# Optimization experiments

Hardware: AMD Instinct MI355X
Metric: run time of the kernel (lower is better)

## Reference

```python
import jax, jax.numpy as jnp
import numpy as np

N_HEADS = 16


def setup_inputs() -> dict:
    key = jax.random.key(0)
    ks = jax.random.split(key, 9)
    B, S, D = 4, 2048, 1024
    query = jax.random.normal(ks[0], (B, S, D), dtype=jnp.float32)
    key_t = jax.random.normal(ks[1], (B, S, D), dtype=jnp.float32)
    value = jax.random.normal(ks[2], (B, S, D), dtype=jnp.float32)
    mask = jax.random.randint(ks[3], (B, 1, S, S), 0, 10) > 0
    scale_w = 0.02  # keep exp(attention) in a safe range
    Wq = jax.random.normal(ks[4], (D, D), dtype=jnp.float32) * scale_w
    Wk = jax.random.normal(ks[5], (D, D), dtype=jnp.float32) * scale_w
    Wv = jax.random.normal(ks[6], (D, D), dtype=jnp.float32) * scale_w
    fc_w = jax.random.normal(ks[7], (D, D), dtype=jnp.float32) * scale_w
    fc_b = jnp.zeros((D,), dtype=jnp.float32)
    return {"query": query, "key": key_t, "value": value, "mask": mask,
            "Wq": Wq, "Wk": Wk, "Wv": Wv, "fc_w": fc_w, "fc_b": fc_b}


def reference(query, key, value, mask, Wq, Wk, Wv, fc_w, fc_b):
    B, S, D = query.shape
    H = N_HEADS
    Dh = D // H
    scale = jnp.sqrt(jnp.asarray(D / H, dtype=query.dtype))
    # Faithful to original: direct reshape [B,S,D] -> [B,H,S,Dh] (no transpose)
    Q = (query @ Wq.T).reshape(B, H, S, Dh)
    K = (key @ Wk.T).reshape(B, H, S, Dh)
    V = (value @ Wv.T).reshape(B, H, S, Dh)
    attn = jnp.einsum('bhqd,bhkd->bhqk', Q, K) / scale  # [B,H,S,S]
    # Hand-rolled masked softmax: exp, masked_fill(False->0), normalize, nan->0
    temp = jnp.where(mask, jnp.exp(attn), 0.0)
    attn = temp / jnp.sum(temp, axis=-1, keepdims=True)
    attn = jnp.where(jnp.isnan(attn), 0.0, attn)
    res = jnp.einsum('bhqk,bhkd->bhqd', attn, V)  # [B,H,S,Dh]
    outs = res.transpose(0, 2, 1, 3).reshape(B, S, D)
    outs = outs @ fc_w.T + fc_b
    return outs, res.transpose(1, 0, 2, 3)
```

## Files before the change

### kernel.cpp

```cpp
#include <hip/hip_runtime.h>


typedef __attribute__((ext_vector_type(8))) short bf16x8;
typedef __attribute__((ext_vector_type(4))) short bf16x4;
typedef __attribute__((ext_vector_type(4))) float f32x4;

#define MFMA32(a, b, c) __builtin_amdgcn_mfma_f32_16x16x32_bf16(a, b, c, 0, 0, 0)

static __device__ __forceinline__ float fast_exp2(float x) {
#if __has_builtin(__builtin_amdgcn_exp2f)
  return __builtin_amdgcn_exp2f(x);
#else
  return __expf(x * 0.69314718056f);
#endif
}

__device__ __forceinline__ unsigned short fbf(float f) {
  union { float f; unsigned u; } x; x.f = f;
  unsigned r = x.u + 0x7fffu + ((x.u >> 16) & 1u);
  return (unsigned short)(r >> 16);
}

static __device__ __forceinline__ bf16x4 pack2(unsigned lo, unsigned hi) {
  union { unsigned u[2]; bf16x4 v; } x; x.u[0] = lo; x.u[1] = hi; return x.v;
}

static __device__ __forceinline__ bf16x8 cat2(bf16x4 lo, bf16x4 hi) {
  union { bf16x4 h[2]; bf16x8 v; } x; x.h[0] = lo; x.h[1] = hi; return x.v;
}

static __device__ __forceinline__ bf16x4 epp(f32x4 s, unsigned pre, int sh) {
  union { float f; unsigned u; } e0, e1, e2, e3;
  e0.f = fast_exp2(s[0]); e1.f = fast_exp2(s[1]);
  e2.f = fast_exp2(s[2]); e3.f = fast_exp2(s[3]);
  unsigned p01 = __builtin_amdgcn_perm(e1.u + 0x8000u, e0.u + 0x8000u, 0x07060302u);
  unsigned p23 = __builtin_amdgcn_perm(e3.u + 0x8000u, e2.u + 0x8000u, 0x07060302u);
  int m0 = __builtin_amdgcn_sbfe(pre, sh + 0, 1), m1 = __builtin_amdgcn_sbfe(pre, sh + 1, 1);
  int m2 = __builtin_amdgcn_sbfe(pre, sh + 2, 1), m3 = __builtin_amdgcn_sbfe(pre, sh + 3, 1);
  unsigned k01 = __builtin_amdgcn_perm((unsigned)m1, (unsigned)m0, 0x07060100u);
  unsigned k23 = __builtin_amdgcn_perm((unsigned)m3, (unsigned)m2, 0x07060100u);
  return pack2(p01 & k01, p23 & k23);
}

__global__ __launch_bounds__(256) void prep_kernel(const float* __restrict__ s0,
                                                   const float* __restrict__ s1,
                                                   const float* __restrict__ s2,
                                                   const float* __restrict__ w0,
                                                   const float* __restrict__ w1,
                                                   const float* __restrict__ w2,
                                                   const float* __restrict__ w3,
                                                   unsigned short* __restrict__ d0,
                                                   unsigned short* __restrict__ d1,
                                                   unsigned short* __restrict__ d2,
                                                   unsigned short* __restrict__ e0,
                                                   unsigned short* __restrict__ e1,
                                                   unsigned short* __restrict__ e2,
                                                   unsigned short* __restrict__ e3) {
  int bid = blockIdx.x;
  const float* s;
  unsigned short* d;
  int i;
  if (bid < 24576) {
    int z = bid >> 13;
    s = (z == 0) ? s0 : (z == 1) ? s1 : s2;
    d = (z == 0) ? d0 : (z == 1) ? d1 : d2;
    i = (bid & 8191) * 256 + threadIdx.x;
  } else {
    int r = bid - 24576;
    int z = r >> 10;
    s = (z == 0) ? w0 : (z == 1) ? w1 : (z == 2) ? w2 : w3;
    d = (z == 0) ? e0 : (z == 1) ? e1 : (z == 2) ? e2 : e3;
    i = (r & 1023) * 256 + threadIdx.x;
  }
  float4 v = ((const float4*)s)[i];
  ushort4 o;
  o.x = fbf(v.x); o.y = fbf(v.y); o.z = fbf(v.z); o.w = fbf(v.w);
  ((ushort4*)d)[i] = o;
}

__global__ __launch_bounds__(256) void pack_mask_kernel(const int* __restrict__ m,
                                                        unsigned long long* __restrict__ o) {
  int i = blockIdx.x * 256 + threadIdx.x;
  unsigned long long b = __ballot(m[i] != 0);
  if ((threadIdx.x & 63) == 0) {
    int row = i >> 11;
    int kt = (i >> 7) & 15;
    int h = (i >> 6) & 1;
    o[(kt * 8192 + row) * 2 + h] = b;
  }
}

__global__ __launch_bounds__(256) void vtrans_kernel(const unsigned short* __restrict__ Vf,
                                                     unsigned short* __restrict__ Vt) {
  __shared__ unsigned short T[64][72];
  const int bh = blockIdx.y;
  const int s0 = blockIdx.x * 64;
  const int tid = threadIdx.x;
  {
    int r = tid >> 2, c = (tid & 3) * 16;
    const unsigned short* src = Vf + bh * 131072 + (s0 + r) * 64 + c;
    uint4 v0 = *(const uint4*)(src);
    uint4 v1 = *(const uint4*)(src + 8);
    *(uint4*)&T[r][c] = v0;
    *(uint4*)&T[r][c + 8] = v1;
  }
  __syncthreads();
  {
    int dh = tid & 63, rb = (tid >> 6) * 16;
    unsigned short o[16];
#pragma unroll
    for (int j = 0; j < 16; ++j) o[j] = T[rb + j][dh];
    unsigned short* dst = Vt + bh * 131072 + dh * 2048 + s0 + rb;
    *(uint4*)dst = *(const uint4*)&o[0];
    *(uint4*)(dst + 8) = *(const uint4*)&o[8];
  }
}

__global__ __launch_bounds__(256) void proj_kernel(const unsigned short* __restrict__ A0,
                                                   const unsigned short* __restrict__ A1,
                                                   const unsigned short* __restrict__ A2,
                                                   const unsigned short* __restrict__ W0,
                                                   const unsigned short* __restrict__ W1,
                                                   const unsigned short* __restrict__ W2,
                                                   unsigned short* __restrict__ C0,
                                                   unsigned short* __restrict__ C1,
                                                   unsigned short* __restrict__ C2) {
  __shared__ unsigned short Alds[128 * 32];
  __shared__ unsigned short Blds[128 * 32];
  const int flat = (blockIdx.z * 64 + blockIdx.y) * 8 + blockIdx.x;
  const int wid = (flat & 7) * 192 + (flat >> 3);
  const int z = wid >> 9;
  const int by = (wid >> 3) & 63;
  const int bx = wid & 7;
  const unsigned short* A = (z == 0) ? A0 : (z == 1) ? A1 : A2;
  const unsigned short* B = (z == 0) ? W0 : (z == 1) ? W1 : W2;
  const int tid = threadIdx.x;
  const int w = tid >> 6, l = tid & 63, q4 = l >> 4, c16 = l & 15;
  const int wm = w & 1, wn = w >> 1;
  const int mBase = by * 128, nBase = bx * 128;

  f32x4 acc[4][4];
#pragma unroll
  for (int a0 = 0; a0 < 4; ++a0)
#pragma unroll
    for (int a1 = 0; a1 < 4; ++a1) acc[a0][a1] = (f32x4){0.f, 0.f, 0.f, 0.f};

  const int r0 = tid >> 2, cc0 = tid & 3;

  for (int kt = 0; kt < 32; ++kt) {
    __syncthreads();
    const unsigned short* ga0 = A + (mBase + r0) * 1024 + kt * 32 + cc0 * 8;
    const unsigned short* ga1 = A + (mBase + 64 + r0) * 1024 + kt * 32 + cc0 * 8;
    const unsigned short* gb0 = B + (nBase + r0) * 1024 + kt * 32 + cc0 * 8;
    const unsigned short* gb1 = B + (nBase + 64 + r0) * 1024 + kt * 32 + cc0 * 8;
    __builtin_amdgcn_global_load_lds((const __attribute__((address_space(1))) void*)ga0,
                                     (__attribute__((address_space(3))) void*)(&Alds[tid * 8]),
                                     16, 0, 0);
    __builtin_amdgcn_global_load_lds((const __attribute__((address_space(1))) void*)ga1,
                                     (__attribute__((address_space(3))) void*)(&Alds[(tid + 256) * 8]),
                                     16, 0, 0);
    __builtin_amdgcn_global_load_lds((const __attribute__((address_space(1))) void*)gb0,
                                     (__attribute__((address_space(3))) void*)(&Blds[tid * 8]),
                                     16, 0, 0);
    __builtin_amdgcn_global_load_lds((const __attribute__((address_space(1))) void*)gb1,
                                     (__attribute__((address_space(3))) void*)(&Blds[(tid + 256) * 8]),
                                     16, 0, 0);
    __syncthreads();

    bf16x8 af[4], bfr[4];
#pragma unroll
    for (int mi = 0; mi < 4; ++mi)
      af[mi] = *(const bf16x8*)&Alds[(wm * 64 + mi * 16 + c16) * 32 + q4 * 8];
#pragma unroll
    for (int ni = 0; ni < 4; ++ni)
      bfr[ni] = *(const bf16x8*)&Blds[(wn * 64 + ni * 16 + c16) * 32 + q4 * 8];
#pragma unroll
    for (int mi = 0; mi < 4; ++mi)
#pragma unroll
      for (int ni = 0; ni < 4; ++ni) acc[mi][ni] = MFMA32(af[mi], bfr[ni], acc[mi][ni]);
  }

  unsigned short* C = (z == 0) ? C0 : (z == 1) ? C1 : C2;
  const float scale = (z == 0) ? 0.18033688f : 1.0f;
#pragma unroll
  for (int mi = 0; mi < 4; ++mi) {
#pragma unroll
    for (int ni = 0; ni < 4; ++ni) {
#pragma unroll
      for (int rg = 0; rg < 4; ++rg) {
        int row = mBase + wm * 64 + mi * 16 + q4 * 4 + rg;
        int col = nBase + wn * 64 + ni * 16 + c16;
        C[row * 1024 + col] = fbf(acc[mi][ni][rg] * scale);
      }
    }
  }
}

__global__ __launch_bounds__(256) void gemm_out(const unsigned short* __restrict__ A,
                                                const unsigned short* __restrict__ B,
                                                float* __restrict__ C,
                                                const float* __restrict__ bias) {
  __shared__ unsigned short Alds[128 * 32];
  __shared__ unsigned short Blds[128 * 32];
  const int flat = blockIdx.y * 8 + blockIdx.x;
  const int wid = (flat & 7) * 64 + (flat >> 3);
  const int by = wid >> 3, bx = wid & 7;
  const int tid = threadIdx.x;
  const int w = tid >> 6, l = tid & 63, q4 = l >> 4, c16 = l & 15;
  const int wm = w & 1, wn = w >> 1;
  const int mBase = by * 128, nBase = bx * 128;

  f32x4 acc[4][4];
#pragma unroll
  for (int a0 = 0; a0 < 4; ++a0)
#pragma unroll
    for (int a1 = 0; a1 < 4; ++a1) acc[a0][a1] = (f32x4){0.f, 0.f, 0.f, 0.f};

  const int r0 = tid >> 2, cc0 = tid & 3;

  for (int kt = 0; kt < 32; ++kt) {
    __syncthreads();
    const unsigned short* ga0 = A + (mBase + r0) * 1024 + kt * 32 + cc0 * 8;
    const unsigned short* ga1 = A + (mBase + 64 + r0) * 1024 + kt * 32 + cc0 * 8;
    const unsigned short* gb0 = B + (nBase + r0) * 1024 + kt * 32 + cc0 * 8;
    const unsigned short* gb1 = B + (nBase + 64 + r0) * 1024 + kt * 32 + cc0 * 8;
    __builtin_amdgcn_global_load_lds((const __attribute__((address_space(1))) void*)ga0,
                                     (__attribute__((address_space(3))) void*)(&Alds[tid * 8]),
                                     16, 0, 0);
    __builtin_amdgcn_global_load_lds((const __attribute__((address_space(1))) void*)ga1,
                                     (__attribute__((address_space(3))) void*)(&Alds[(tid + 256) * 8]),
                                     16, 0, 0);
    __builtin_amdgcn_global_load_lds((const __attribute__((address_space(1))) void*)gb0,
                                     (__attribute__((address_space(3))) void*)(&Blds[tid * 8]),
                                     16, 0, 0);
    __builtin_amdgcn_global_load_lds((const __attribute__((address_space(1))) void*)gb1,
                                     (__attribute__((address_space(3))) void*)(&Blds[(tid + 256) * 8]),
                                     16, 0, 0);
    __syncthreads();

    bf16x8 af[4], bfr[4];
#pragma unroll
    for (int mi = 0; mi < 4; ++mi)
      af[mi] = *(const bf16x8*)&Alds[(wm * 64 + mi * 16 + c16) * 32 + q4 * 8];
#pragma unroll
    for (int ni = 0; ni < 4; ++ni)
      bfr[ni] = *(const bf16x8*)&Blds[(wn * 64 + ni * 16 + c16) * 32 + q4 * 8];
#pragma unroll
    for (int mi = 0; mi < 4; ++mi)
#pragma unroll
      for (int ni = 0; ni < 4; ++ni) acc[mi][ni] = MFMA32(af[mi], bfr[ni], acc[mi][ni]);
  }

#pragma unroll
  for (int mi = 0; mi < 4; ++mi) {
#pragma unroll
    for (int ni = 0; ni < 4; ++ni) {
#pragma unroll
      for (int rg = 0; rg < 4; ++rg) {
        int row = mBase + wm * 64 + mi * 16 + q4 * 4 + rg;
        int col = nBase + wn * 64 + ni * 16 + c16;
        C[row * 1024 + col] = acc[mi][ni][rg] + bias[col];
      }
    }
  }
}

__global__ __launch_bounds__(256, 4) void flash_kernel(const unsigned short* __restrict__ Q,
                                                       const unsigned short* __restrict__ K,
                                                       const unsigned short* __restrict__ Vt,
                                                       const uint4* __restrict__ mb,
                                                       unsigned short* __restrict__ Cws,
                                                       float* __restrict__ res2) {
  __shared__ unsigned short Klds[128 * 64];
  __shared__ unsigned short Vtlds[64 * 128];
  const int tid = threadIdx.x;
  const int w = tid >> 6, l = tid & 63, q4 = l >> 4, c16 = l & 15;
  const int q44 = q4 * 4;
  const int flat = (blockIdx.z * 16 + blockIdx.y) * 16 + blockIdx.x;
  const int wid = (flat & 7) * 128 + (flat >> 3);
  const int qt = wid & 15, h = (wid >> 4) & 15, b = wid >> 8;
  const unsigned short* Qh = Q + (b * 2048 + h * 128) * 1024;
  const unsigned short* Kh = K + (b * 2048 + h * 128) * 1024;
  const unsigned short* Vth = Vt + (b * 16 + h) * 64 * 2048;

  bf16x8 qf[2][2];
#pragma unroll
  for (int i = 0; i < 2; ++i)
#pragma unroll
    for (int kc = 0; kc < 2; ++kc)
      qf[i][kc] = *(const bf16x8*)(Qh + (qt * 128 + w * 32 + i * 16 + c16) * 64 + kc * 32 + q4 * 8);

  const int rowi = b * 2048 + qt * 128 + w * 32 + c16;

  const int kOff = (tid >> 3) * 64 + (((tid & 7) ^ ((tid >> 3) & 7)) * 8);
  const int vOff = (tid >> 4) * 2048 + (((tid & 15) ^ (tid >> 4)) * 8);

  const int kb0 = c16 * 64 + ((q4 ^ (c16 & 7)) * 8);
  const int kb1 = kb0 ^ 32;
  const int vb = c16 * 128 + (q4 & 1) * 4;
  const int q41 = q4 >> 1;

  const bf16x8 ones8 = {(short)0x3F80, (short)0x3F80, (short)0x3F80, (short)0x3F80,
                        (short)0x3F80, (short)0x3F80, (short)0x3F80, (short)0x3F80};

  f32x4 oacc[2][4], soacc[2];
#pragma unroll
  for (int i = 0; i < 2; ++i) {
    soacc[i] = (f32x4){0.f, 0.f, 0.f, 0.f};
#pragma unroll
    for (int t = 0; t < 4; ++t) oacc[i][t] = (f32x4){0.f, 0.f, 0.f, 0.f};
  }

  for (int kt = 0; kt < 16; ++kt) {
    const unsigned short* gk = Kh + kt * 8192 + kOff;
    const unsigned short* gv = Vth + kt * 128 + vOff;
#pragma unroll
    for (int j = 0; j < 4; ++j) {
      __builtin_amdgcn_global_load_lds((const __attribute__((address_space(1))) void*)(gk + j * 2048),
                                       (__attribute__((address_space(3))) void*)(&Klds[(j * 256 + tid) * 8]),
                                       16, 0, 0);
      __builtin_amdgcn_global_load_lds((const __attribute__((address_space(1))) void*)(gv + j * 32768),
                                       (__attribute__((address_space(3))) void*)(&Vtlds[(j * 256 + tid) * 8]),
                                       16, 0, 0);
    }
    uint4 m0 = mb[kt * 8192 + rowi];
    uint4 m1 = mb[kt * 8192 + rowi + 16];
    unsigned pre0[4] = {m0.x >> q44, m0.y >> q44, m0.z >> q44, m0.w >> q44};
    unsigned pre1[4] = {m1.x >> q44, m1.y >> q44, m1.z >> q44, m1.w >> q44};
    __syncthreads();

#pragma unroll
    for (int m = 0; m < 4; ++m) {
      bf16x8 kfE0 = *(const bf16x8*)(Klds + kb0 + (2 * m) * 1024);
      bf16x8 kfE1 = *(const bf16x8*)(Klds + kb1 + (2 * m) * 1024);
      bf16x8 kfO0 = *(const bf16x8*)(Klds + kb0 + (2 * m + 1) * 1024);
      bf16x8 kfO1 = *(const bf16x8*)(Klds + kb1 + (2 * m + 1) * 1024);
      f32x4 sE0 = {0.f, 0.f, 0.f, 0.f}, sE1 = {0.f, 0.f, 0.f, 0.f};
      f32x4 sO0 = {0.f, 0.f, 0.f, 0.f}, sO1 = {0.f, 0.f, 0.f, 0.f};
      __builtin_amdgcn_s_setprio(1);
      sE0 = MFMA32(kfE0, qf[0][0], sE0); sE0 = MFMA32(kfE1, qf[0][1], sE0);
      sE1 = MFMA32(kfE0, qf[1][0], sE1); sE1 = MFMA32(kfE1, qf[1][1], sE1);
      sO0 = MFMA32(kfO0, qf[0][0], sO0); sO0 = MFMA32(kfO1, qf[0][1], sO0);
      sO1 = MFMA32(kfO0, qf[1][0], sO1); sO1 = MFMA32(kfO1, qf[1][1], sO1);
      __builtin_amdgcn_s_setprio(0);

      int shE = 0, shO = 16;
      bf16x8 pf0 = cat2(epp(sE0, pre0[m], shE), epp(sO0, pre0[m], shO));
      bf16x8 pf1 = cat2(epp(sE1, pre1[m], shE), epp(sO1, pre1[m], shO));

      int pLo = (4 * m + q41) ^ c16;
      int aLo = vb + pLo * 8;
      __builtin_amdgcn_s_setprio(1);
#pragma unroll
      for (int t = 0; t < 4; ++t) {
        bf16x4 vlo = *(const bf16x4*)(Vtlds + aLo + t * 2048);
        bf16x4 vhi = *(const bf16x4*)(Vtlds + (aLo ^ 16) + t * 2048);
        bf16x8 vf8 = cat2(vlo, vhi);
        oacc[0][t] = MFMA32(vf8, pf0, oacc[0][t]);
        oacc[1][t] = MFMA32(vf8, pf1, oacc[1][t]);
      }
      soacc[0] = MFMA32(ones8, pf0, soacc[0]);
      soacc[1] = MFMA32(ones8, pf1, soacc[1]);
      __builtin_amdgcn_s_setprio(0);
    }
    __syncthreads();
  }

#pragma unroll
  for (int i = 0; i < 2; ++i) {
    float sum = soacc[i][0];
    float rcp = (sum > 0.f) ? (1.0f / sum) : 0.f;
    int q = qt * 128 + w * 32 + i * 16 + c16;
    float* rp = res2 + (((h * 4 + b) * 2048 + q) * 64 + q44);
    unsigned short* cp = Cws + ((b * 2048 + q) * 1024 + h * 64 + q44);
#pragma unroll
    for (int t = 0; t < 4; ++t) {
      float o0 = oacc[i][t][0] * rcp, o1 = oacc[i][t][1] * rcp;
      float o2 = oacc[i][t][2] * rcp, o3 = oacc[i][t][3] * rcp;
      float4 fo = {o0, o1, o2, o3};
      *(float4*)(rp + t * 16) = fo;
      ushort4 cv = {fbf(o0), fbf(o1), fbf(o2), fbf(o3)};
      *(ushort4*)(cp + t * 16) = cv;
    }
  }
}

extern "C" void kernel_launch(void* const* d_in, const int* in_sizes, int n_in,
                              void* d_out, int out_size, void* d_ws, size_t ws_size,
                              hipStream_t stream) {
  const float* query = (const float*)d_in[0];
  const float* key_t = (const float*)d_in[1];
  const float* value = (const float*)d_in[2];
  const int* mask = (const int*)d_in[3];
  const float* Wq = (const float*)d_in[4];
  const float* Wk = (const float*)d_in[5];
  const float* Wv = (const float*)d_in[6];
  const float* fcw = (const float*)d_in[7];
  const float* fcb = (const float*)d_in[8];
  float* out = (float*)d_out;

  char* ws = (char*)d_ws;
  unsigned short* qbf = (unsigned short*)(ws);
  unsigned short* kbf = (unsigned short*)(ws + (16u << 20));
  unsigned short* vbf = (unsigned short*)(ws + (32u << 20));
  unsigned short* wqb = (unsigned short*)(ws + (48u << 20));
  unsigned short* wkb = (unsigned short*)(ws + (50u << 20));
  unsigned short* wvb = (unsigned short*)(ws + (52u << 20));
  unsigned short* fwb = (unsigned short*)(ws + (54u << 20));
  unsigned short* Qf = (unsigned short*)(ws + (56u << 20));
  unsigned short* Kf = (unsigned short*)(ws + (72u << 20));
  unsigned short* Vnat = (unsigned short*)(ws + (88u << 20));
  unsigned short* Cws = qbf;
  unsigned long long* mbits = (unsigned long long*)kbf;
  unsigned short* Vt = vbf;

  prep_kernel<<<28672, 256, 0, stream>>>(query, key_t, value, Wq, Wk, Wv, fcw,
                                         qbf, kbf, vbf, wqb, wkb, wvb, fwb);

  proj_kernel<<<dim3(8, 64, 3), 256, 0, stream>>>(qbf, kbf, vbf, wqb, wkb, wvb,
                                                  Qf, Kf, Vnat);

  vtrans_kernel<<<dim3(32, 64), 256, 0, stream>>>(Vnat, Vt);

  pack_mask_kernel<<<65536, 256, 0, stream>>>(mask, mbits);

  flash_kernel<<<dim3(16, 16, 4), 256, 0, stream>>>(Qf, Kf, Vt, (const uint4*)mbits, Cws,
                                                    out + 8388608);

  gemm_out<<<dim3(8, 64), 256, 0, stream>>>(Cws, fwb, out, fcb);
}
```

Measured before the change: 407.3 us.

## Double GEMM K-tile to 64 with XOR-swizzled LDS; drop setprio in attention

The projection and output GEMMs now stage a 64-wide K tile per iteration instead of 32. This halves the number of barrier-separated load phases and runs two MFMA sub-steps per tile. Global-to-LDS loads use an XOR swizzle on the 16-byte chunk index, and fragment reads apply the matching swizzle to avoid LDS bank conflicts with the longer 128-byte rows. The attention kernel's s_setprio calls around its MFMA blocks are removed. The cost is doubled LDS usage per block, which may reduce occupancy.

```diff
diff --git a/kernel.cpp b/kernel.cpp
--- a/kernel.cpp
+++ b/kernel.cpp
@@ -6,6 +6,10 @@
 typedef __attribute__((ext_vector_type(4))) float f32x4;
 
 #define MFMA32(a, b, c) __builtin_amdgcn_mfma_f32_16x16x32_bf16(a, b, c, 0, 0, 0)
+
+#define GLDS16(g, l)                                                                       \
+  __builtin_amdgcn_global_load_lds((const __attribute__((address_space(1))) void*)(g),     \
+                                   (__attribute__((address_space(3))) void*)(l), 16, 0, 0)
 
 static __device__ __forceinline__ float fast_exp2(float x) {
 #if __has_builtin(__builtin_amdgcn_exp2f)
@@ -125,8 +129,8 @@
                                                    unsigned short* __restrict__ C0,
                                                    unsigned short* __restrict__ C1,
                                                    unsigned short* __restrict__ C2) {
-  __shared__ unsigned short Alds[128 * 32];
-  __shared__ unsigned short Blds[128 * 32];
+  __shared__ unsigned short Alds[128 * 64];
+  __shared__ unsigned short Blds[128 * 64];
   const int flat = (blockIdx.z * 64 + blockIdx.y) * 8 + blockIdx.x;
   const int wid = (flat & 7) * 192 + (flat >> 3);
   const int z = wid >> 9;
@@ -145,39 +149,38 @@
 #pragma unroll
     for (int a1 = 0; a1 < 4; ++a1) acc[a0][a1] = (f32x4){0.f, 0.f, 0.f, 0.f};
 
-  const int r0 = tid >> 2, cc0 = tid & 3;
-
-  for (int kt = 0; kt < 32; ++kt) {
-    __syncthreads();
-    const unsigned short* ga0 = A + (mBase + r0) * 1024 + kt * 32 + cc0 * 8;
-    const unsigned short* ga1 = A + (mBase + 64 + r0) * 1024 + kt * 32 + cc0 * 8;
-    const unsigned short* gb0 = B + (nBase + r0) * 1024 + kt * 32 + cc0 * 8;
-    const unsigned short* gb1 = B + (nBase + 64 + r0) * 1024 + kt * 32 + cc0 * 8;
-    __builtin_amdgcn_global_load_lds((const __attribute__((address_space(1))) void*)ga0,
-                                     (__attribute__((address_space(3))) void*)(&Alds[tid * 8]),
-                                     16, 0, 0);
-    __builtin_amdgcn_global_load_lds((const __attribute__((address_space(1))) void*)ga1,
-                                     (__attribute__((address_space(3))) void*)(&Alds[(tid + 256) * 8]),
-                                     16, 0, 0);
-    __builtin_amdgcn_global_load_lds((const __attribute__((address_space(1))) void*)gb0,
-                                     (__attribute__((address_space(3))) void*)(&Blds[tid * 8]),
-                                     16, 0, 0);
-    __builtin_amdgcn_global_load_lds((const __attribute__((address_space(1))) void*)gb1,
-                                     (__attribute__((address_space(3))) void*)(&Blds[(tid + 256) * 8]),
-                                     16, 0, 0);
-    __syncthreads();
-
-    bf16x8 af[4], bfr[4];
-#pragma unroll
-    for (int mi = 0; mi < 4; ++mi)
-      af[mi] = *(const bf16x8*)&Alds[(wm * 64 + mi * 16 + c16) * 32 + q4 * 8];
-#pragma unroll
-    for (int ni = 0; ni < 4; ++ni)
-      bfr[ni] = *(const bf16x8*)&Blds[(wn * 64 + ni * 16 + c16) * 32 + q4 * 8];
-#pragma unroll
-    for (int mi = 0; mi < 4; ++mi)
-#pragma unroll
-      for (int ni = 0; ni < 4; ++ni) acc[mi][ni] = MFMA32(af[mi], bfr[ni], acc[mi][ni]);
+  const int rsub = tid >> 3;
+  const int csw = ((tid & 7) ^ (rsub & 7)) * 8;
+
+  for (int kt = 0; kt < 16; ++kt) {
+    __syncthreads();
+#pragma unroll
+    for (int j = 0; j < 4; ++j) {
+      const unsigned short* gA = A + (mBase + j * 32 + rsub) * 1024 + kt * 64 + csw;
+      const unsigned short* gB = B + (nBase + j * 32 + rsub) * 1024 + kt * 64 + csw;
+      GLDS16(gA, &Alds[(j * 256 + tid) * 8]);
+      GLDS16(gB, &Blds[(j * 256 + tid) * 8]);
+    }
+    __syncthreads();
+
+#pragma unroll
+    for (int kk = 0; kk < 2; ++kk) {
+      bf16x8 af[4], bfr[4];
+#pragma unroll
+      for (int mi = 0; mi < 4; ++mi) {
+        int row = wm * 64 + mi * 16 + c16;
+        af[mi] = *(const bf16x8*)&Alds[(row * 64 + ((q4 ^ (c16 & 7)) * 8)) ^ (kk << 5)];
+      }
+#pragma unroll
+      for (int ni = 0; ni < 4; ++ni) {
+        int row = wn * 64 + ni * 16 + c16;
+        bfr[ni] = *(const bf16x8*)&Blds[(row * 64 + ((q4 ^ (c16 & 7)) * 8)) ^ (kk << 5)];
+      }
+#pragma unroll
+      for (int mi = 0; mi < 4; ++mi)
+#pragma unroll
+        for (int ni = 0; ni < 4; ++ni) acc[mi][ni] = MFMA32(af[mi], bfr[ni], acc[mi][ni]);
+    }
   }
 
   unsigned short* C = (z == 0) ? C0 : (z == 1) ? C1 : C2;
@@ -200,8 +203,8 @@
                                                 const unsigned short* __restrict__ B,
                                                 float* __restrict__ C,
                                                 const float* __restrict__ bias) {
-  __shared__ unsigned short Alds[128 * 32];
-  __shared__ unsigned short Blds[128 * 32];
+  __shared__ unsigned short Alds[128 * 64];
+  __shared__ unsigned short Blds[128 * 64];
   const int flat = blockIdx.y * 8 + blockIdx.x;
   const int wid = (flat & 7) * 64 + (flat >> 3);
   const int by = wid >> 3, bx = wid & 7;
@@ -216,39 +219,38 @@
 #pragma unroll
     for (int a1 = 0; a1 < 4; ++a1) acc[a0][a1] = (f32x4){0.f, 0.f, 0.f, 0.f};
 
-  const int r0 = tid >> 2, cc0 = tid & 3;
-
-  for (int kt = 0; kt < 32; ++kt) {
-    __syncthreads();
-    const unsigned short* ga0 = A + (mBase + r0) * 1024 + kt * 32 + cc0 * 8;
-    const unsigned short* ga1 = A + (mBase + 64 + r0) * 1024 + kt * 32 + cc0 * 8;
-    const unsigned short* gb0 = B + (nBase + r0) * 1024 + kt * 32 + cc0 * 8;
-    const unsigned short* gb1 = B + (nBase + 64 + r0) * 1024 + kt * 32 + cc0 * 8;
-    __builtin_amdgcn_global_load_lds((const __attribute__((address_space(1))) void*)ga0,
-                                     (__attribute__((address_space(3))) void*)(&Alds[tid * 8]),
-                                     16, 0, 0);
-    __builtin_amdgcn_global_load_lds((const __attribute__((address_space(1))) void*)ga1,
-                                     (__attribute__((address_space(3))) void*)(&Alds[(tid + 256) * 8]),
-                                     16, 0, 0);
-    __builtin_amdgcn_global_load_lds((const __attribute__((address_space(1))) void*)gb0,
-                                     (__attribute__((address_space(3))) void*)(&Blds[tid * 8]),
-                                     16, 0, 0);
-    __builtin_amdgcn_global_load_lds((const __attribute__((address_space(1))) void*)gb1,
-                                     (__attribute__((address_space(3))) void*)(&Blds[(tid + 256) * 8]),
-                                     16, 0, 0);
-    __syncthreads();
-
-    bf16x8 af[4], bfr[4];
-#pragma unroll
-    for (int mi = 0; mi < 4; ++mi)
-      af[mi] = *(const bf16x8*)&Alds[(wm * 64 + mi * 16 + c16) * 32 + q4 * 8];
-#pragma unroll
-    for (int ni = 0; ni < 4; ++ni)
-      bfr[ni] = *(const bf16x8*)&Blds[(wn * 64 + ni * 16 + c16) * 32 + q4 * 8];
-#pragma unroll
-    for (int mi = 0; mi < 4; ++mi)
-#pragma unroll
-      for (int ni = 0; ni < 4; ++ni) acc[mi][ni] = MFMA32(af[mi], bfr[ni], acc[mi][ni]);
+  const int rsub = tid >> 3;
+  const int csw = ((tid & 7) ^ (rsub & 7)) * 8;
+
+  for (int kt = 0; kt < 16; ++kt) {
+    __syncthreads();
+#pragma unroll
+    for (int j = 0; j < 4; ++j) {
+      const unsigned short* gA = A + (mBase + j * 32 + rsub) * 1024 + kt * 64 + csw;
+      const unsigned short* gB = B + (nBase + j * 32 + rsub) * 1024 + kt * 64 + csw;
+      GLDS16(gA, &Alds[(j * 256 + tid) * 8]);
+      GLDS16(gB, &Blds[(j * 256 + tid) * 8]);
+    }
+    __syncthreads();
+
+#pragma unroll
+    for (int kk = 0; kk < 2; ++kk) {
+      bf16x8 af[4], bfr[4];
+#pragma unroll
+      for (int mi = 0; mi < 4; ++mi) {
+        int row = wm * 64 + mi * 16 + c16;
+        af[mi] = *(const bf16x8*)&Alds[(row * 64 + ((q4 ^ (c16 & 7)) * 8)) ^ (kk << 5)];
+      }
+#pragma unroll
+      for (int ni = 0; ni < 4; ++ni) {
+        int row = wn * 64 + ni * 16 + c16;
+        bfr[ni] = *(const bf16x8*)&Blds[(row * 64 + ((q4 ^ (c16 & 7)) * 8)) ^ (kk << 5)];
+      }
+#pragma unroll
+      for (int mi = 0; mi < 4; ++mi)
+#pragma unroll
+        for (int ni = 0; ni < 4; ++ni) acc[mi][ni] = MFMA32(af[mi], bfr[ni], acc[mi][ni]);
+    }
   }
 
 #pragma unroll
@@ -316,12 +318,8 @@
     const unsigned short* gv = Vth + kt * 128 + vOff;
 #pragma unroll
     for (int j = 0; j < 4; ++j) {
-      __builtin_amdgcn_global_load_lds((const __attribute__((address_space(1))) void*)(gk + j * 2048),
-                                       (__attribute__((address_space(3))) void*)(&Klds[(j * 256 + tid) * 8]),
-                                       16, 0, 0);
-      __builtin_amdgcn_global_load_lds((const __attribute__((address_space(1))) void*)(gv + j * 32768),
-                                       (__attribute__((address_space(3))) void*)(&Vtlds[(j * 256 + tid) * 8]),
-                                       16, 0, 0);
+      GLDS16(gk + j * 2048, &Klds[(j * 256 + tid) * 8]);
+      GLDS16(gv + j * 32768, &Vtlds[(j * 256 + tid) * 8]);
     }
     uint4 m0 = mb[kt * 8192 + rowi];
     uint4 m1 = mb[kt * 8192 + rowi + 16];
@@ -337,12 +335,10 @@
       bf16x8 kfO1 = *(const bf16x8*)(Klds + kb1 + (2 * m + 1) * 1024);
       f32x4 sE0 = {0.f, 0.f, 0.f, 0.f}, sE1 = {0.f, 0.f, 0.f, 0.f};
       f32x4 sO0 = {0.f, 0.f, 0.f, 0.f}, sO1 = {0.f, 0.f, 0.f, 0.f};
-      __builtin_amdgcn_s_setprio(1);
       sE0 = MFMA32(kfE0, qf[0][0], sE0); sE0 = MFMA32(kfE1, qf[0][1], sE0);
       sE1 = MFMA32(kfE0, qf[1][0], sE1); sE1 = MFMA32(kfE1, qf[1][1], sE1);
       sO0 = MFMA32(kfO0, qf[0][0], sO0); sO0 = MFMA32(kfO1, qf[0][1], sO0);
       sO1 = MFMA32(kfO0, qf[1][0], sO1); sO1 = MFMA32(kfO1, qf[1][1], sO1);
-      __builtin_amdgcn_s_setprio(0);
 
       int shE = 0, shO = 16;
       bf16x8 pf0 = cat2(epp(sE0, pre0[m], shE), epp(sO0, pre0[m], shO));
@@ -350,7 +346,6 @@
 
       int pLo = (4 * m + q41) ^ c16;
       int aLo = vb + pLo * 8;
-      __builtin_amdgcn_s_setprio(1);
 #pragma unroll
       for (int t = 0; t < 4; ++t) {
         bf16x4 vlo = *(const bf16x4*)(Vtlds + aLo + t * 2048);
@@ -361,7 +356,6 @@
       }
       soacc[0] = MFMA32(ones8, pf0, soacc[0]);
       soacc[1] = MFMA32(ones8, pf1, soacc[1]);
-      __builtin_amdgcn_s_setprio(0);
     }
     __syncthreads();
   }
```

Result: no change. 409.2 us (+0.5%).
